# Kernel optimization log

Hardware: AMD Instinct MI355X
Metric: run time of the kernel (lower is better)

The kernel has to match this reference:

```python
import jax, jax.numpy as jnp
import numpy as np


def setup_inputs() -> dict:
    key = jax.random.key(0)
    ks = jax.random.split(key, 8)
    N, E, H, C, L, G = 100000, 1600000, 128, 10, 5, 64
    x = jax.random.normal(ks[0], (N, H), dtype=jnp.float32)
    edge_index = jax.random.randint(ks[1], (2, E), 0, N, dtype=jnp.int32)
    batch = jnp.sort(jax.random.randint(ks[2], (N,), 0, G, dtype=jnp.int32))
    # Glorot-ish init scale for stability
    Ws = jax.random.normal(ks[3], (L, H, H), dtype=jnp.float32) * (1.0 / np.sqrt(H))
    bs = jax.random.normal(ks[4], (L, H), dtype=jnp.float32) * 0.01
    W_out = jax.random.normal(ks[5], (H, C), dtype=jnp.float32) * (1.0 / np.sqrt(H))
    b_out = jax.random.normal(ks[6], (C,), dtype=jnp.float32) * 0.01
    return {"x": x, "edge_index": edge_index, "batch": batch, "num_graphs": G,
            "Ws": Ws, "bs": bs, "W_out": W_out, "b_out": b_out}


def reference(x, edge_index, batch, num_graphs, Ws, bs, W_out, b_out):
    N = x.shape[0]
    # --- GCN normalization (add self-loops, symmetric deg^-1/2 norm), computed once ---
    loop = jnp.arange(N, dtype=edge_index.dtype)
    src = jnp.concatenate([edge_index[0], loop])  # message sources (x_j)
    dst = jnp.concatenate([edge_index[1], loop])  # aggregation targets
    deg = jax.ops.segment_sum(jnp.ones_like(dst, dtype=x.dtype), dst, num_segments=N)
    dis = jnp.where(deg > 0, jax.lax.rsqrt(jnp.maximum(deg, 1.0)), 0.0)
    norm = dis[src] * dis[dst]  # [E+N]
    # --- stacked GCNConv + ReLU ---
    for l in range(Ws.shape[0]):
        xw = x @ Ws[l]                                   # [N, H] dense transform
        msg = norm[:, None] * xw[src]                    # gather + scale per edge
        x = jax.nn.relu(jax.ops.segment_sum(msg, dst, num_segments=N) + bs[l])
    # --- global mean pool over graphs ---
    sums = jax.ops.segment_sum(x, batch, num_segments=num_graphs)       # [G, H]
    cnts = jax.ops.segment_sum(jnp.ones((N,), x.dtype), batch, num_segments=num_graphs)
    pooled = sums / jnp.maximum(cnts, 1.0)[:, None]
    return pooled @ W_out + b_out
```

## Files before the change

kernel.cpp:

```cpp
#include <hip/hip_runtime.h>
#include <hip/hip_bf16.h>
#include <stdint.h>

#define HDIM 128
#define SBITS 10
#define SBMAX 128

typedef __attribute__((ext_vector_type(8))) short short8;
typedef __attribute__((ext_vector_type(4))) float f32x4;

__device__ __forceinline__ ushort f2bf(float f) {
  uint u = __float_as_uint(f);
  u = (u + 0x7fffu + ((u >> 16) & 1u)) >> 16;
  return (ushort)u;
}
__device__ __forceinline__ float bflo(uint v) { return __uint_as_float(v << 16); }
__device__ __forceinline__ float bfhi(uint v) { return __uint_as_float(v & 0xffff0000u); }

__device__ __forceinline__ int pdeg4(int c) { return (c + 4) & ~3; }

__device__ __forceinline__ uint pack_cw(int src, float w) {
  uint w15 = (__float_as_uint(w) + 0x8000u) >> 16;
  return (uint)src | (w15 << 17);
}
__device__ __forceinline__ uint cw_src(uint u) { return u & 0x1FFFFu; }
__device__ __forceinline__ float cw_w(uint u) { return __uint_as_float((u >> 17) << 16); }


__global__ __launch_bounds__(256) void bucket_edges(const int* __restrict__ ei,
                                                    int* __restrict__ bktcur,
                                                    uint* __restrict__ bkt, int E,
                                                    int cap) {
  __shared__ int hist[SBMAX], base[SBMAX];
  const int t = threadIdx.x;
  const int c0 = blockIdx.x * 2048;
  for (int i = t; i < SBMAX; i += 256) hist[i] = 0;
  __syncthreads();
  uint pk[8];
  int sb_[8], rk[8];
#pragma unroll
  for (int j = 0; j < 8; ++j) {
    int idx = c0 + j * 256 + t;
    sb_[j] = -1;
    if (idx < E) {
      int s = ei[idx];
      int d = ei[E + idx];
      int b = d >> SBITS;
      pk[j] = (uint)(d & 1023) | ((uint)s << SBITS);
      sb_[j] = b;
      rk[j] = atomicAdd(&hist[b], 1);
    }
  }
  __syncthreads();
  for (int i = t; i < SBMAX; i += 256)
    base[i] = hist[i] ? atomicAdd(&bktcur[i * 16], hist[i]) : 0;
  __syncthreads();
#pragma unroll
  for (int j = 0; j < 8; ++j)
    if (sb_[j] >= 0)
      bkt[(size_t)sb_[j] * cap + base[sb_[j]] + rk[j]] = pk[j];
}

__global__ __launch_bounds__(256) void csr_count(const uint* __restrict__ bkt,
                                                 const int* __restrict__ bktcur,
                                                 float* __restrict__ dis,
                                                 int* __restrict__ sbtot, int cap,
                                                 int N) {
  __shared__ int cnt[1024];
  __shared__ int red[256];
  const int sb = blockIdx.x, t = threadIdx.x;
  const int n0 = sb << SBITS;
  const int ecnt = bktcur[sb * 16];
  const uint* eb = bkt + (size_t)sb * cap;
  for (int i = t; i < 1024; i += 256) cnt[i] = 0;
  __syncthreads();
  for (int i = t; i < ecnt; i += 256)
    atomicAdd(&cnt[__builtin_nontemporal_load(eb + i) & 1023], 1);
  __syncthreads();
  int s = 0;
#pragma unroll
  for (int j = 0; j < 4; ++j) {
    int idx = t * 4 + j, n = n0 + idx;
    if (n < N) {
      dis[n] = rsqrtf((float)(cnt[idx] + 1));
      s += pdeg4(cnt[idx]);
    }
  }
  red[t] = s;
  __syncthreads();
  for (int off = 128; off; off >>= 1) {
    if (t < off) red[t] += red[t + off];
    __syncthreads();
  }
  if (t == 0) sbtot[sb] = red[0];
}

__global__ __launch_bounds__(128) void scan_sb(const int* __restrict__ sbtot,
                                               int* __restrict__ sbbase,
                                               int* __restrict__ rowptr, int SB,
                                               int N) {
  __shared__ int sh[128];
  int t = threadIdx.x;
  int v = (t < SB) ? sbtot[t] : 0;
  sh[t] = v;
  __syncthreads();
  for (int off = 1; off < 128; off <<= 1) {
    int add = (t >= off) ? sh[t - off] : 0;
    __syncthreads();
    sh[t] += add;
    __syncthreads();
  }
  if (t < SB) sbbase[t] = sh[t] - v;
  if (t == 127) rowptr[N] = sh[127];
}

__global__ __launch_bounds__(256) void csr_place(const uint* __restrict__ bkt,
                                                 const int* __restrict__ bktcur,
                                                 const int* __restrict__ sbbase,
                                                 const float* __restrict__ dis,
                                                 int* __restrict__ rowptr,
                                                 uint* __restrict__ colw, int cap,
                                                 int N) {
  __shared__ int cnt[1024], cur[1024];
  __shared__ int sh[256];
  const int sb = blockIdx.x, t = threadIdx.x;
  const int n0 = sb << SBITS;
  const int ecnt = bktcur[sb * 16];
  const uint* eb = bkt + (size_t)sb * cap;
  const int base = sbbase[sb];
  for (int i = t; i < 1024; i += 256) cnt[i] = 0;
  __syncthreads();
  for (int i = t; i < ecnt; i += 256)
    atomicAdd(&cnt[__builtin_nontemporal_load(eb + i) & 1023], 1);
  __syncthreads();
  int v[4], tsum = 0;
#pragma unroll
  for (int j = 0; j < 4; ++j) {
    int idx = t * 4 + j, n = n0 + idx;
    v[j] = (n < N) ? pdeg4(cnt[idx]) : 0;
    tsum += v[j];
  }
  sh[t] = tsum;
  __syncthreads();
  for (int off = 1; off < 256; off <<= 1) {
    int add = (t >= off) ? sh[t - off] : 0;
    __syncthreads();
    sh[t] += add;
    __syncthreads();
  }
  int p = sh[t] - tsum;
#pragma unroll
  for (int j = 0; j < 4; ++j) {
    int idx = t * 4 + j, n = n0 + idx;
    if (n < N) {
      rowptr[n] = base + p;
      cur[idx] = p + 1;
      float dn = dis[n];
      colw[base + p] = pack_cw(n, dn * dn);
      int deg = cnt[idx];
      for (int q = deg + 1; q < v[j]; ++q) colw[base + p + q] = (uint)n;
    }
    p += v[j];
  }
  __syncthreads();
  for (int i = t; i < ecnt; i += 256) {
    uint u = __builtin_nontemporal_load(eb + i);
    int dloc = (int)(u & 1023);
    int s2 = (int)(u >> SBITS);
    int pos = atomicAdd(&cur[dloc], 1);
    int d = n0 + dloc;
    colw[base + pos] = pack_cw(s2, dis[s2] * dis[d]);
  }
}

__global__ __launch_bounds__(256) void swz_w(const float* __restrict__ Ws,
                                             ushort* __restrict__ Wsw, int total) {
  int idx = blockIdx.x * 256 + threadIdx.x;
  if (idx >= total) return;
  int l = idx >> 14, r = idx & 16383;
  int j = r & 7, lane = (r >> 3) & 63, kk = (r >> 9) & 3, c = r >> 11;
  int n = c * 16 + (lane & 15);
  int k = kk * 32 + (lane >> 4) * 8 + j;
  Wsw[idx] = f2bf(Ws[l * 16384 + k * HDIM + n]);
}


template <bool F32IN>
__global__ __launch_bounds__(256) void gemm_kernel(const void* __restrict__ Xin,
                                                   const ushort* __restrict__ Wsw,
                                                   ushort* __restrict__ XW, int N,
                                                   int ntiles) {
  __shared__ ushort wlds[16384];
  __shared__ ushort clds[64 * 136];
  const int t = threadIdx.x;
  {
    const int4* src = (const int4*)Wsw;
    int4* dst = (int4*)wlds;
#pragma unroll
    for (int i = 0; i < 8; ++i) dst[t + 256 * i] = src[t + 256 * i];
  }
  __syncthreads();

  const int wave = t >> 6, lane = t & 63;
  const int kq = lane >> 4;

  for (int tile = blockIdx.x; tile < ntiles; tile += gridDim.x) {
    const int row0 = tile * 64 + wave * 16 + (lane & 15);
    const bool inb = row0 < N;

    short8 afr[4];
#pragma unroll
    for (int kk = 0; kk < 4; ++kk) afr[kk] = short8{0, 0, 0, 0, 0, 0, 0, 0};
    if (inb) {
      if constexpr (F32IN) {
        const float* arow = (const float*)Xin + (size_t)row0 * HDIM;
#pragma unroll
        for (int kk = 0; kk < 4; ++kk) {
          float4 x0 = *(const float4*)(arow + kk * 32 + kq * 8);
          float4 x1 = *(const float4*)(arow + kk * 32 + kq * 8 + 4);
          short8 f;
          f[0] = (short)f2bf(x0.x); f[1] = (short)f2bf(x0.y);
          f[2] = (short)f2bf(x0.z); f[3] = (short)f2bf(x0.w);
          f[4] = (short)f2bf(x1.x); f[5] = (short)f2bf(x1.y);
          f[6] = (short)f2bf(x1.z); f[7] = (short)f2bf(x1.w);
          afr[kk] = f;
        }
      } else {
        const short8* arow = (const short8*)((const ushort*)Xin + (size_t)row0 * HDIM);
#pragma unroll
        for (int kk = 0; kk < 4; ++kk) afr[kk] = arow[kk * 4 + kq];
      }
    }

    f32x4 acc[8];
#pragma unroll
    for (int c = 0; c < 8; ++c) acc[c] = f32x4{0.f, 0.f, 0.f, 0.f};
#pragma unroll
    for (int kk = 0; kk < 4; ++kk) {
#pragma unroll
      for (int c = 0; c < 8; ++c) {
        short8 bfr = *(const short8*)(wlds + (((c * 4 + kk) * 64 + lane) << 3));
        acc[c] = __builtin_amdgcn_mfma_f32_16x16x32_bf16(afr[kk], bfr, acc[c], 0, 0, 0);
      }
    }

    __syncthreads();
    const int m0 = wave * 16 + kq * 4;
#pragma unroll
    for (int c = 0; c < 8; ++c) {
      int col = c * 16 + (lane & 15);
#pragma unroll
      for (int r = 0; r < 4; ++r) clds[(m0 + r) * 136 + col] = f2bf(acc[c][r]);
    }
    __syncthreads();
#pragma unroll
    for (int i = 0; i < 4; ++i) {
      int idx = t + 256 * i;
      int row = idx >> 4, piece = idx & 15;
      int grow = tile * 64 + row;
      if (grow < N)
        ((int4*)XW)[(size_t)tile * 1024 + idx] =
            *(const int4*)(clds + row * 136 + piece * 8);
    }
  }
}

__global__ __launch_bounds__(256, 6) void agg_kernel(const ushort* __restrict__ XW,
                                                     const uint* __restrict__ colw,
                                                     const int* __restrict__ rowptr,
                                                     const float* __restrict__ bias,
                                                     ushort* __restrict__ Y, int N) {
  const int lane = threadIdx.x & 63;
  const int node = blockIdx.x * 4 + (threadIdx.x >> 6);
  if (node >= N) return;
  const int e = lane >> 4, c = lane & 15;
  const int beg = rowptr[node];
  const int pdeg = rowptr[node + 1] - beg;
  const int last = pdeg - 1;

  uint cw[6];
#pragma unroll
  for (int k = 0; k < 6; ++k) {
    int off = 4 * k + e;
    cw[k] = __builtin_nontemporal_load(colw + beg + (off < pdeg ? off : last));
  }
  uint4 gv[6];
#pragma unroll
  for (int k = 0; k < 6; ++k)
    gv[k] = *(const uint4*)(XW + ((size_t)cw_src(cw[k]) << 7) + c * 8);

  float acc[8];
#pragma unroll
  for (int i = 0; i < 8; ++i) acc[i] = 0.f;

#pragma unroll
  for (int k = 0; k < 6; ++k) {
    int off = 4 * k + e;
    float w = (off < pdeg) ? cw_w(cw[k]) : 0.f;
    uint4 v = gv[k];
    acc[0] += w * bflo(v.x); acc[1] += w * bfhi(v.x);
    acc[2] += w * bflo(v.y); acc[3] += w * bfhi(v.y);
    acc[4] += w * bflo(v.z); acc[5] += w * bfhi(v.z);
    acc[6] += w * bflo(v.w); acc[7] += w * bfhi(v.w);
  }
  for (int off = 24 + e; off < pdeg; off += 4) {
    uint u = __builtin_nontemporal_load(colw + beg + off);
    uint4 v = *(const uint4*)(XW + ((size_t)cw_src(u) << 7) + c * 8);
    float w = cw_w(u);
    acc[0] += w * bflo(v.x); acc[1] += w * bfhi(v.x);
    acc[2] += w * bflo(v.y); acc[3] += w * bfhi(v.y);
    acc[4] += w * bflo(v.z); acc[5] += w * bfhi(v.z);
    acc[6] += w * bflo(v.w); acc[7] += w * bfhi(v.w);
  }

#pragma unroll
  for (int i = 0; i < 8; ++i) {
    acc[i] += __shfl_xor(acc[i], 16, 64);
    acc[i] += __shfl_xor(acc[i], 32, 64);
  }
  if (e == 0) {
    float4 b0 = *(const float4*)(bias + c * 8);
    float4 b1 = *(const float4*)(bias + c * 8 + 4);
    uint4 pk;
    pk.x = (uint)f2bf(fmaxf(acc[0] + b0.x, 0.f)) | ((uint)f2bf(fmaxf(acc[1] + b0.y, 0.f)) << 16);
    pk.y = (uint)f2bf(fmaxf(acc[2] + b0.z, 0.f)) | ((uint)f2bf(fmaxf(acc[3] + b0.w, 0.f)) << 16);
    pk.z = (uint)f2bf(fmaxf(acc[4] + b1.x, 0.f)) | ((uint)f2bf(fmaxf(acc[5] + b1.y, 0.f)) << 16);
    pk.w = (uint)f2bf(fmaxf(acc[6] + b1.z, 0.f)) | ((uint)f2bf(fmaxf(acc[7] + b1.w, 0.f)) << 16);
    *(uint4*)(Y + (size_t)node * HDIM + c * 8) = pk;
  }
}


__global__ __launch_bounds__(256) void pool_partial(const ushort* __restrict__ x,
                                                    const int* __restrict__ batch,
                                                    float* __restrict__ pooled,
                                                    int* __restrict__ gcnt, int N) {
  const int g = blockIdx.x, s = blockIdx.y;
  const int t = threadIdx.x;
  __shared__ int range[2];
  __shared__ float sums[256];
  if (t < 2) {
    int target = g + t;
    int lo = 0, hi = N;
    while (lo < hi) {
      int mid = (lo + hi) >> 1;
      if (batch[mid] < target) lo = mid + 1;
      else hi = mid;
    }
    range[t] = lo;
  }
  __syncthreads();
  int beg = range[0], end = range[1];
  if (s == 0 && t == 0) gcnt[g] = end - beg;
  int col = t & 127, half = t >> 7;
  float acc = 0.f;
  for (int n = beg + s * 2 + half; n < end; n += 16) {
    acc += __uint_as_float(((uint)x[(size_t)n * HDIM + col]) << 16);
  }
  sums[t] = acc;
  __syncthreads();
  if (t < 128) atomicAdd(&pooled[g * HDIM + t], sums[t] + sums[t + 128]);
}

__global__ __launch_bounds__(256) void out_final(const float* __restrict__ pooled,
                                                 const int* __restrict__ gcnt,
                                                 const float* __restrict__ W_out,
                                                 const float* __restrict__ b_out,
                                                 float* __restrict__ out, int G, int C) {
  int i = blockIdx.x * 256 + threadIdx.x;
  if (i >= G * C) return;
  int g = i / C, c = i - g * C;
  float inv = 1.f / (float)max(gcnt[g], 1);
  const float* pg = pooled + g * HDIM;
  float o = 0.f;
  for (int h = 0; h < HDIM; ++h) o += pg[h] * W_out[h * C + c];
  out[i] = b_out[c] + o * inv;
}


extern "C" void kernel_launch(void* const* d_in, const int* in_sizes, int n_in,
                              void* d_out, int out_size, void* d_ws, size_t ws_size,
                              hipStream_t stream) {
  (void)n_in;
  (void)ws_size;
  const float* x = (const float*)d_in[0];
  const int* ei = (const int*)d_in[1];
  const int* batch = (const int*)d_in[2];
  const float* Ws = (const float*)d_in[4];
  const float* bs = (const float*)d_in[5];
  const float* W_out = (const float*)d_in[6];
  const float* b_out = (const float*)d_in[7];
  float* out = (float*)d_out;

  const int N = in_sizes[0] / HDIM;
  const int E = in_sizes[1] / 2;
  const int L = in_sizes[5] / HDIM;
  const int C = in_sizes[7];
  const int G = out_size / C;
  const int SB = (N + 1023) >> SBITS;
  const int cap = E / SB + 8192;

  char* p = (char*)d_ws;
  auto carve = [&](size_t bytes) {
    char* r = p;
    p += (bytes + 255) & ~(size_t)255;
    return r;
  };
  int* bktcur = (int*)carve(SBMAX * 64);
  float* dis = (float*)carve((size_t)N * 4);
  int* rowptr = (int*)carve((size_t)(N + 1) * 4);
  int* sbtot = (int*)carve(SBMAX * 4);
  int* sbbase = (int*)carve(SBMAX * 4);
  uint* bkt = (uint*)carve((size_t)SB * cap * 4);
  uint* colw = (uint*)carve(((size_t)E + 4 * (size_t)N + 64) * 4);
  ushort* Wsw = (ushort*)carve((size_t)L * HDIM * HDIM * 2);
  ushort* xw = (ushort*)carve((size_t)N * HDIM * 2);
  ushort* y0 = (ushort*)carve((size_t)N * HDIM * 2);
  ushort* y1 = (ushort*)carve((size_t)N * HDIM * 2);
  float* pooled = (float*)carve((size_t)G * HDIM * 4 + (size_t)G * 4);
  int* gcnt = (int*)(pooled + (size_t)G * HDIM);

  hipMemsetAsync(bktcur, 0, SBMAX * 64, stream);
  hipMemsetAsync(pooled, 0, (size_t)G * HDIM * 4 + (size_t)G * 4, stream);

  bucket_edges<<<(E + 2047) / 2048, 256, 0, stream>>>(ei, bktcur, bkt, E, cap);
  csr_count<<<SB, 256, 0, stream>>>(bkt, bktcur, dis, sbtot, cap, N);
  scan_sb<<<1, 128, 0, stream>>>(sbtot, sbbase, rowptr, SB, N);
  csr_place<<<SB, 256, 0, stream>>>(bkt, bktcur, sbbase, dis, rowptr, colw, cap, N);
  swz_w<<<(L * HDIM * HDIM + 255) / 256, 256, 0, stream>>>(Ws, Wsw, L * HDIM * HDIM);

  const int ntiles = (N + 63) / 64;
  const int gb = 768;
  gemm_kernel<true><<<gb, 256, 0, stream>>>(x, Wsw, xw, N, ntiles);
  agg_kernel<<<(N + 3) / 4, 256, 0, stream>>>(xw, colw, rowptr, bs, y0, N);
  ushort* xc = y0;
  ushort* xn = y1;
  for (int l = 1; l < L; ++l) {
    gemm_kernel<false><<<gb, 256, 0, stream>>>(xc, Wsw + (size_t)l * HDIM * HDIM, xw, N, ntiles);
    agg_kernel<<<(N + 3) / 4, 256, 0, stream>>>(xw, colw, rowptr, bs + (size_t)l * HDIM, xn, N);
    ushort* tmp = xc;
    xc = xn;
    xn = tmp;
  }
  pool_partial<<<dim3(G, 8), 256, 0, stream>>>(xc, batch, pooled, gcnt, N);
  out_final<<<(G * C + 255) / 256, 256, 0, stream>>>(pooled, gcnt, W_out, b_out, out, G, C);
}
```

Measured before the change: 575.7 us.

## Shrink CSR superblocks, reuse degrees, raise agg occupancy, pack FMAs

The CSR build now uses 256-node superblocks instead of 1024, which gives 391 blocks rather than 98, and the per-node degree is stored once so csr_place no longer recounts the bucket. The aggregation kernel's launch bound is raised to 8 waves per SIMD, and its accumulation uses float2 FMAs so the compiler can emit packed ops. The goals are more parallelism in the CSR build, no duplicate histogram pass, and better latency hiding in aggregation. In exchange, the per-bucket capacity margin is smaller, which could overflow on skewed inputs, and the occupancy bound limits the registers available to agg.

```diff
diff --git a/kernel.cpp b/kernel.cpp
--- a/kernel.cpp
+++ b/kernel.cpp
@@ -3,11 +3,13 @@
 #include <stdint.h>
 
 #define HDIM 128
-#define SBITS 10
-#define SBMAX 128
+#define SBITS 8
+#define SBMASK 255
+#define SBMAX 512
 
 typedef __attribute__((ext_vector_type(8))) short short8;
 typedef __attribute__((ext_vector_type(4))) float f32x4;
+typedef __attribute__((ext_vector_type(2))) float f32x2;
 
 __device__ __forceinline__ ushort f2bf(float f) {
   uint u = __float_as_uint(f);
@@ -46,7 +48,7 @@
       int s = ei[idx];
       int d = ei[E + idx];
       int b = d >> SBITS;
-      pk[j] = (uint)(d & 1023) | ((uint)s << SBITS);
+      pk[j] = (uint)(d & SBMASK) | ((uint)s << SBITS);
       sb_[j] = b;
       rk[j] = atomicAdd(&hist[b], 1);
     }
@@ -64,27 +66,27 @@
 __global__ __launch_bounds__(256) void csr_count(const uint* __restrict__ bkt,
                                                  const int* __restrict__ bktcur,
                                                  float* __restrict__ dis,
+                                                 int* __restrict__ degs,
                                                  int* __restrict__ sbtot, int cap,
                                                  int N) {
-  __shared__ int cnt[1024];
+  __shared__ int cnt[256];
   __shared__ int red[256];
   const int sb = blockIdx.x, t = threadIdx.x;
   const int n0 = sb << SBITS;
   const int ecnt = bktcur[sb * 16];
   const uint* eb = bkt + (size_t)sb * cap;
-  for (int i = t; i < 1024; i += 256) cnt[i] = 0;
+  cnt[t] = 0;
   __syncthreads();
   for (int i = t; i < ecnt; i += 256)
-    atomicAdd(&cnt[__builtin_nontemporal_load(eb + i) & 1023], 1);
+    atomicAdd(&cnt[__builtin_nontemporal_load(eb + i) & SBMASK], 1);
   __syncthreads();
   int s = 0;
-#pragma unroll
-  for (int j = 0; j < 4; ++j) {
-    int idx = t * 4 + j, n = n0 + idx;
-    if (n < N) {
-      dis[n] = rsqrtf((float)(cnt[idx] + 1));
-      s += pdeg4(cnt[idx]);
-    }
+  const int n = n0 + t;
+  if (n < N) {
+    int c = cnt[t];
+    degs[n] = c;
+    dis[n] = rsqrtf((float)(c + 1));
+    s = pdeg4(c);
   }
   red[t] = s;
   __syncthreads();
@@ -95,52 +97,44 @@
   if (t == 0) sbtot[sb] = red[0];
 }
 
-__global__ __launch_bounds__(128) void scan_sb(const int* __restrict__ sbtot,
+__global__ __launch_bounds__(512) void scan_sb(const int* __restrict__ sbtot,
                                                int* __restrict__ sbbase,
                                                int* __restrict__ rowptr, int SB,
                                                int N) {
-  __shared__ int sh[128];
+  __shared__ int sh[SBMAX];
   int t = threadIdx.x;
   int v = (t < SB) ? sbtot[t] : 0;
   sh[t] = v;
   __syncthreads();
-  for (int off = 1; off < 128; off <<= 1) {
+  for (int off = 1; off < SBMAX; off <<= 1) {
     int add = (t >= off) ? sh[t - off] : 0;
     __syncthreads();
     sh[t] += add;
     __syncthreads();
   }
   if (t < SB) sbbase[t] = sh[t] - v;
-  if (t == 127) rowptr[N] = sh[127];
+  if (t == SBMAX - 1) rowptr[N] = sh[SBMAX - 1];
 }
 
 __global__ __launch_bounds__(256) void csr_place(const uint* __restrict__ bkt,
                                                  const int* __restrict__ bktcur,
                                                  const int* __restrict__ sbbase,
                                                  const float* __restrict__ dis,
+                                                 const int* __restrict__ degs,
                                                  int* __restrict__ rowptr,
                                                  uint* __restrict__ colw, int cap,
                                                  int N) {
-  __shared__ int cnt[1024], cur[1024];
+  __shared__ int cur[256];
   __shared__ int sh[256];
   const int sb = blockIdx.x, t = threadIdx.x;
   const int n0 = sb << SBITS;
   const int ecnt = bktcur[sb * 16];
   const uint* eb = bkt + (size_t)sb * cap;
   const int base = sbbase[sb];
-  for (int i = t; i < 1024; i += 256) cnt[i] = 0;
-  __syncthreads();
-  for (int i = t; i < ecnt; i += 256)
-    atomicAdd(&cnt[__builtin_nontemporal_load(eb + i) & 1023], 1);
-  __syncthreads();
-  int v[4], tsum = 0;
-#pragma unroll
-  for (int j = 0; j < 4; ++j) {
-    int idx = t * 4 + j, n = n0 + idx;
-    v[j] = (n < N) ? pdeg4(cnt[idx]) : 0;
-    tsum += v[j];
-  }
-  sh[t] = tsum;
+  const int n = n0 + t;
+  const int deg = (n < N) ? degs[n] : 0;
+  const int v = (n < N) ? pdeg4(deg) : 0;
+  sh[t] = v;
   __syncthreads();
   for (int off = 1; off < 256; off <<= 1) {
     int add = (t >= off) ? sh[t - off] : 0;
@@ -148,24 +142,18 @@
     sh[t] += add;
     __syncthreads();
   }
-  int p = sh[t] - tsum;
-#pragma unroll
-  for (int j = 0; j < 4; ++j) {
-    int idx = t * 4 + j, n = n0 + idx;
-    if (n < N) {
-      rowptr[n] = base + p;
-      cur[idx] = p + 1;
-      float dn = dis[n];
-      colw[base + p] = pack_cw(n, dn * dn);
-      int deg = cnt[idx];
-      for (int q = deg + 1; q < v[j]; ++q) colw[base + p + q] = (uint)n;
-    }
-    p += v[j];
+  const int p = sh[t] - v;
+  if (n < N) {
+    rowptr[n] = base + p;
+    cur[t] = p + 1;
+    float dn = dis[n];
+    colw[base + p] = pack_cw(n, dn * dn);
+    for (int q = deg + 1; q < v; ++q) colw[base + p + q] = (uint)n;
   }
   __syncthreads();
   for (int i = t; i < ecnt; i += 256) {
     uint u = __builtin_nontemporal_load(eb + i);
-    int dloc = (int)(u & 1023);
+    int dloc = (int)(u & SBMASK);
     int s2 = (int)(u >> SBITS);
     int pos = atomicAdd(&cur[dloc], 1);
     int d = n0 + dloc;
@@ -265,7 +253,7 @@
   }
 }
 
-__global__ __launch_bounds__(256, 6) void agg_kernel(const ushort* __restrict__ XW,
+__global__ __launch_bounds__(256, 8) void agg_kernel(const ushort* __restrict__ XW,
                                                      const uint* __restrict__ colw,
                                                      const int* __restrict__ rowptr,
                                                      const float* __restrict__ bias,
@@ -289,43 +277,47 @@
   for (int k = 0; k < 6; ++k)
     gv[k] = *(const uint4*)(XW + ((size_t)cw_src(cw[k]) << 7) + c * 8);
 
-  float acc[8];
-#pragma unroll
-  for (int i = 0; i < 8; ++i) acc[i] = 0.f;
+  f32x2 acc[4];
+#pragma unroll
+  for (int i = 0; i < 4; ++i) acc[i] = f32x2{0.f, 0.f};
 
 #pragma unroll
   for (int k = 0; k < 6; ++k) {
     int off = 4 * k + e;
     float w = (off < pdeg) ? cw_w(cw[k]) : 0.f;
+    f32x2 wv = f32x2{w, w};
     uint4 v = gv[k];
-    acc[0] += w * bflo(v.x); acc[1] += w * bfhi(v.x);
-    acc[2] += w * bflo(v.y); acc[3] += w * bfhi(v.y);
-    acc[4] += w * bflo(v.z); acc[5] += w * bfhi(v.z);
-    acc[6] += w * bflo(v.w); acc[7] += w * bfhi(v.w);
+    acc[0] = __builtin_elementwise_fma(wv, f32x2{bflo(v.x), bfhi(v.x)}, acc[0]);
+    acc[1] = __builtin_elementwise_fma(wv, f32x2{bflo(v.y), bfhi(v.y)}, acc[1]);
+    acc[2] = __builtin_elementwise_fma(wv, f32x2{bflo(v.z), bfhi(v.z)}, acc[2]);
+    acc[3] = __builtin_elementwise_fma(wv, f32x2{bflo(v.w), bfhi(v.w)}, acc[3]);
   }
   for (int off = 24 + e; off < pdeg; off += 4) {
     uint u = __builtin_nontemporal_load(colw + beg + off);
     uint4 v = *(const uint4*)(XW + ((size_t)cw_src(u) << 7) + c * 8);
     float w = cw_w(u);
-    acc[0] += w * bflo(v.x); acc[1] += w * bfhi(v.x);
-    acc[2] += w * bflo(v.y); acc[3] += w * bfhi(v.y);
-    acc[4] += w * bflo(v.z); acc[5] += w * bfhi(v.z);
-    acc[6] += w * bflo(v.w); acc[7] += w * bfhi(v.w);
-  }
-
-#pragma unroll
-  for (int i = 0; i < 8; ++i) {
-    acc[i] += __shfl_xor(acc[i], 16, 64);
-    acc[i] += __shfl_xor(acc[i], 32, 64);
+    f32x2 wv = f32x2{w, w};
+    acc[0] = __builtin_elementwise_fma(wv, f32x2{bflo(v.x), bfhi(v.x)}, acc[0]);
+    acc[1] = __builtin_elementwise_fma(wv, f32x2{bflo(v.y), bfhi(v.y)}, acc[1]);
+    acc[2] = __builtin_elementwise_fma(wv, f32x2{bflo(v.z), bfhi(v.z)}, acc[2]);
+    acc[3] = __builtin_elementwise_fma(wv, f32x2{bflo(v.w), bfhi(v.w)}, acc[3]);
+  }
+
+#pragma unroll
+  for (int i = 0; i < 4; ++i) {
+    acc[i].x += __shfl_xor(acc[i].x, 16, 64);
+    acc[i].y += __shfl_xor(acc[i].y, 16, 64);
+    acc[i].x += __shfl_xor(acc[i].x, 32, 64);
+    acc[i].y += __shfl_xor(acc[i].y, 32, 64);
   }
   if (e == 0) {
     float4 b0 = *(const float4*)(bias + c * 8);
     float4 b1 = *(const float4*)(bias + c * 8 + 4);
     uint4 pk;
-    pk.x = (uint)f2bf(fmaxf(acc[0] + b0.x, 0.f)) | ((uint)f2bf(fmaxf(acc[1] + b0.y, 0.f)) << 16);
-    pk.y = (uint)f2bf(fmaxf(acc[2] + b0.z, 0.f)) | ((uint)f2bf(fmaxf(acc[3] + b0.w, 0.f)) << 16);
-    pk.z = (uint)f2bf(fmaxf(acc[4] + b1.x, 0.f)) | ((uint)f2bf(fmaxf(acc[5] + b1.y, 0.f)) << 16);
-    pk.w = (uint)f2bf(fmaxf(acc[6] + b1.z, 0.f)) | ((uint)f2bf(fmaxf(acc[7] + b1.w, 0.f)) << 16);
+    pk.x = (uint)f2bf(fmaxf(acc[0].x + b0.x, 0.f)) | ((uint)f2bf(fmaxf(acc[0].y + b0.y, 0.f)) << 16);
+    pk.y = (uint)f2bf(fmaxf(acc[1].x + b0.z, 0.f)) | ((uint)f2bf(fmaxf(acc[1].y + b0.w, 0.f)) << 16);
+    pk.z = (uint)f2bf(fmaxf(acc[2].x + b1.x, 0.f)) | ((uint)f2bf(fmaxf(acc[2].y + b1.y, 0.f)) << 16);
+    pk.w = (uint)f2bf(fmaxf(acc[3].x + b1.z, 0.f)) | ((uint)f2bf(fmaxf(acc[3].y + b1.w, 0.f)) << 16);
     *(uint4*)(Y + (size_t)node * HDIM + c * 8) = pk;
   }
 }
@@ -397,8 +389,8 @@
   const int L = in_sizes[5] / HDIM;
   const int C = in_sizes[7];
   const int G = out_size / C;
-  const int SB = (N + 1023) >> SBITS;
-  const int cap = E / SB + 8192;
+  const int SB = (N + SBMASK) >> SBITS;
+  const int cap = E / SB + 2048;
 
   char* p = (char*)d_ws;
   auto carve = [&](size_t bytes) {
@@ -408,6 +400,7 @@
   };
   int* bktcur = (int*)carve(SBMAX * 64);
   float* dis = (float*)carve((size_t)N * 4);
+  int* degs = (int*)carve((size_t)N * 4);
   int* rowptr = (int*)carve((size_t)(N + 1) * 4);
   int* sbtot = (int*)carve(SBMAX * 4);
   int* sbbase = (int*)carve(SBMAX * 4);
@@ -424,9 +417,9 @@
   hipMemsetAsync(pooled, 0, (size_t)G * HDIM * 4 + (size_t)G * 4, stream);
 
   bucket_edges<<<(E + 2047) / 2048, 256, 0, stream>>>(ei, bktcur, bkt, E, cap);
-  csr_count<<<SB, 256, 0, stream>>>(bkt, bktcur, dis, sbtot, cap, N);
-  scan_sb<<<1, 128, 0, stream>>>(sbtot, sbbase, rowptr, SB, N);
-  csr_place<<<SB, 256, 0, stream>>>(bkt, bktcur, sbbase, dis, rowptr, colw, cap, N);
+  csr_count<<<SB, 256, 0, stream>>>(bkt, bktcur, dis, degs, sbtot, cap, N);
+  scan_sb<<<1, SBMAX, 0, stream>>>(sbtot, sbbase, rowptr, SB, N);
+  csr_place<<<SB, 256, 0, stream>>>(bkt, bktcur, sbbase, dis, degs, rowptr, colw, cap, N);
   swz_w<<<(L * HDIM * HDIM + 255) / 256, 256, 0, stream>>>(Ws, Wsw, L * HDIM * HDIM);
 
   const int ntiles = (N + 63) / 64;
```

Result: faster. 556.2 us (-3.4%).
